# Optimization experiments

Hardware: AMD Instinct MI355X
Metric: run time of the kernel (lower is better)

Reference implementation:

```python
import jax, jax.numpy as jnp
import numpy as np
import math

N_NODES = 50000
N_EDGES = 800000
D_NODE = 128
D_EDGE = 64  # 4 + dist_embed_dim(60)
N_HEADS = 8
HEAD_DIM = D_NODE // N_HEADS


def setup_inputs() -> dict:
    key = jax.random.key(0)
    ks = jax.random.split(key, 8)
    scale_q = 1.0 / math.sqrt(D_NODE)
    scale_kv = 1.0 / math.sqrt(D_NODE + D_EDGE)
    return {
        "node_feats": jax.random.normal(ks[0], (N_NODES, D_NODE), jnp.float32),
        "edge_feats": jax.random.normal(ks[1], (N_EDGES, D_EDGE), jnp.float32),
        "edge_index": jax.random.randint(ks[2], (2, N_EDGES), 0, N_NODES, jnp.int32),
        "Wq": jax.random.normal(ks[3], (D_NODE, D_NODE), jnp.float32) * scale_q,
        "bq": jnp.zeros((D_NODE,), jnp.float32),
        "Wk": jax.random.normal(ks[4], (D_NODE + D_EDGE, D_NODE), jnp.float32) * scale_kv,
        "bk": jnp.zeros((D_NODE,), jnp.float32),
        "Wv": jax.random.normal(ks[5], (D_NODE + D_EDGE, D_NODE), jnp.float32) * scale_kv,
        "bv": jnp.zeros((D_NODE,), jnp.float32),
        "Wo": jax.random.normal(ks[6], (D_NODE, D_NODE), jnp.float32) * scale_q,
        "bo": jnp.zeros((D_NODE,), jnp.float32),
    }


def reference(node_feats, edge_feats, edge_index, Wq, bq, Wk, bk, Wv, bv, Wo, bo):
    src, tgt = edge_index[0], edge_index[1]
    n = node_feats.shape[0]
    e = edge_feats.shape[0]

    # per-edge Q from target node, K/V from [source node || edge feats]
    q = (node_feats[tgt] @ Wq + bq).reshape(e, N_HEADS, HEAD_DIM)
    kv_input = jnp.concatenate([node_feats[src], edge_feats], axis=-1)  # [E, D_NODE+D_EDGE]
    k = (kv_input @ Wk + bk).reshape(e, N_HEADS, HEAD_DIM)
    v = (kv_input @ Wv + bv).reshape(e, N_HEADS, HEAD_DIM)

    # per-edge attention logits [E, H]
    a = jnp.einsum("ehc,ehc->eh", q, k) / math.sqrt(HEAD_DIM)

    # segment softmax over edges grouped by target node (numerically stable)
    seg_max = jax.ops.segment_max(a, tgt, num_segments=n)      # [N, H]
    a = jnp.exp(a - seg_max[tgt])
    seg_sum = jax.ops.segment_sum(a, tgt, num_segments=n)      # [N, H]
    a = a / seg_sum[tgt]

    # weighted scatter-sum aggregate
    o = jax.ops.segment_sum(a[..., None] * v, tgt, num_segments=n)  # [N, H, C]
    out = o.reshape(n, N_HEADS * HEAD_DIM) @ Wo + bo
    return out  # dropout is identity at inference
```

## Files before the change

### kernel.cpp

```cpp
#include <hip/hip_runtime.h>

#define NND 50000
#define NED 800000
#define DN 128
#define DE 64
#define DKV 192
#define NH 8
#define HD 16

__device__ __forceinline__ float sane(float x) {
    return (x == x && fabsf(x) < 1e30f) ? x : 0.f;
}

__global__ __launch_bounds__(256) void node_proj_qkv(
    const float* __restrict__ nf,
    const float* __restrict__ Wq, const float* __restrict__ bq,
    const float* __restrict__ Wk, const float* __restrict__ bk,
    const float* __restrict__ Wv, const float* __restrict__ bv,
    float* __restrict__ Qn, float* __restrict__ Kn, float* __restrict__ Vn)
{
    __shared__ alignas(16) float xs[128][8];
    const int t = threadIdx.x;
    const int nb = blockIdx.x * 8;
    {
        const int node = t >> 5;
        const int k0 = (t & 31) * 4;
        const float4 x4 = *(const float4*)(nf + (size_t)(nb + node) * DN + k0);
        xs[k0 + 0][node] = x4.x;
        xs[k0 + 1][node] = x4.y;
        xs[k0 + 2][node] = x4.z;
        xs[k0 + 3][node] = x4.w;
    }
    __syncthreads();

    const int col = t & 127;
    const int grp = t >> 7;
    float aq[4], ak[4], av[4];
    const float bqv = bq[col], bkv = bk[col], bvv = bv[col];
#pragma unroll
    for (int i = 0; i < 4; i++) { aq[i] = bqv; ak[i] = bkv; av[i] = bvv; }

#pragma unroll 4
    for (int k = 0; k < 128; k++) {
        const float wq = Wq[k * DN + col];
        const float wk = Wk[k * DN + col];
        const float wv = Wv[k * DN + col];
        const float4 x = *(const float4*)&xs[k][grp * 4];
        aq[0] += x.x * wq; aq[1] += x.y * wq; aq[2] += x.z * wq; aq[3] += x.w * wq;
        ak[0] += x.x * wk; ak[1] += x.y * wk; ak[2] += x.z * wk; ak[3] += x.w * wk;
        av[0] += x.x * wv; av[1] += x.y * wv; av[2] += x.z * wv; av[3] += x.w * wv;
    }
#pragma unroll
    for (int i = 0; i < 4; i++) {
        const size_t r = (size_t)(nb + grp * 4 + i) * DN + col;
        Qn[r] = aq[i]; Kn[r] = ak[i]; Vn[r] = av[i];
    }
}

__global__ __launch_bounds__(256) void node_proj_q(
    const float* __restrict__ nf,
    const float* __restrict__ Wq, const float* __restrict__ bq,
    float* __restrict__ Qn)
{
    __shared__ alignas(16) float xs[128][8];
    const int t = threadIdx.x;
    const int nb = blockIdx.x * 8;
    {
        const int node = t >> 5;
        const int k0 = (t & 31) * 4;
        const float4 x4 = *(const float4*)(nf + (size_t)(nb + node) * DN + k0);
        xs[k0 + 0][node] = x4.x;
        xs[k0 + 1][node] = x4.y;
        xs[k0 + 2][node] = x4.z;
        xs[k0 + 3][node] = x4.w;
    }
    __syncthreads();

    const int col = t & 127;
    const int grp = t >> 7;
    float aq[4];
    const float bqv = bq[col];
#pragma unroll
    for (int i = 0; i < 4; i++) aq[i] = bqv;

#pragma unroll 4
    for (int k = 0; k < 128; k++) {
        const float wq = Wq[k * DN + col];
        const float4 x = *(const float4*)&xs[k][grp * 4];
        aq[0] += x.x * wq; aq[1] += x.y * wq; aq[2] += x.z * wq; aq[3] += x.w * wq;
    }
#pragma unroll
    for (int i = 0; i < 4; i++)
        Qn[(size_t)(nb + grp * 4 + i) * DN + col] = aq[i];
}

__global__ __launch_bounds__(256) void edge_hist(
    const int* __restrict__ eidx, int* __restrict__ cnt)
{
    const int e = blockIdx.x * 256 + threadIdx.x;
    atomicAdd(&cnt[eidx[NED + e]], 1);
}

__global__ __launch_bounds__(1024) void scan_offsets(
    const int* __restrict__ cnt, int* __restrict__ offs)
{
    __shared__ int partial[1024];
    const int t = threadIdx.x;
    constexpr int CH = (NND + 1023) / 1024;
    const int base = t * CH;
    int s = 0;
    for (int i = 0; i < CH; i++) {
        const int idx = base + i;
        if (idx < NND) s += cnt[idx];
    }
    partial[t] = s;
    __syncthreads();
    for (int off = 1; off < 1024; off <<= 1) {
        const int v = (t >= off) ? partial[t - off] : 0;
        __syncthreads();
        partial[t] += v;
        __syncthreads();
    }
    int run = (t == 0) ? 0 : partial[t - 1];
    for (int i = 0; i < CH; i++) {
        const int idx = base + i;
        if (idx < NND) { offs[idx] = run; run += cnt[idx]; }
    }
}

__global__ __launch_bounds__(256) void edge_scatter(
    const int* __restrict__ eidx, int* __restrict__ offs,
    int* __restrict__ perm, int* __restrict__ srcp)
{
    const int e = blockIdx.x * 256 + threadIdx.x;
    const int pos = atomicAdd(&offs[eidx[NED + e]], 1);
    perm[pos] = e;
    srcp[pos] = eidx[e];
}

__global__ __launch_bounds__(256) void edge_aggregate(
    const float* __restrict__ ef,
    const int* __restrict__ cnt, const int* __restrict__ offs,
    const int* __restrict__ perm, const int* __restrict__ srcp,
    const float* __restrict__ Wk, const float* __restrict__ Wv,
    const float* __restrict__ Kn, const float* __restrict__ Vn,
    float* qo)
{
    __shared__ alignas(16) float efs[4][8][64];
    const int t = threadIdx.x;
    const int w = t >> 6;
    const int l = t & 63;
    const int j = l & 7;
    const int node = blockIdx.x * 4 + w;

    const int end = offs[node];
    const int beg = end - cnt[node];

    const float* __restrict__ WkB = Wk + 128 * DN;
    const float* __restrict__ WvB = Wv + 128 * DN;

    const float2 q2 = *(const float2*)(qo + (size_t)node * DN + 2 * l);

    float qt[8];
#pragma unroll
    for (int i = 0; i < 8; i++) qt[i] = 0.f;
#pragma unroll 16
    for (int k = 0; k < 64; k++) {
        const float2 wk2 = *(const float2*)(WkB + k * DN + 2 * l);
        float part = q2.x * wk2.x + q2.y * wk2.y;
        part += __shfl_xor(part, 1);
        part += __shfl_xor(part, 2);
        part += __shfl_xor(part, 4);
        if (j == (k >> 3)) qt[k & 7] = part;
    }

    float acc0 = 0.f, acc1 = 0.f, segacc = 0.f;
    float gt[8];
#pragma unroll
    for (int i = 0; i < 8; i++) gt[i] = 0.f;

    for (int base = beg; base < end; base += 8) {
        const int myE = min(base + (l >> 3), end - 1);
        const int pe = perm[myE];
        const float4 A = *(const float4*)(ef + (size_t)pe * DE + j * 8);
        const float4 B = *(const float4*)(ef + (size_t)pe * DE + j * 8 + 4);
        *(float4*)&efs[w][l >> 3][j * 8]     = A;
        *(float4*)&efs[w][l >> 3][j * 8 + 4] = B;

        const int mySrc = srcp[myE];

#pragma unroll
        for (int e = 0; e < 8; e++) {
            const int se = __builtin_amdgcn_readlane(mySrc, e * 8);
            const float4 efA = *(const float4*)&efs[w][e][j * 8];
            const float4 efB = *(const float4*)&efs[w][e][j * 8 + 4];
            const float2 kn2 = *(const float2*)(Kn + (size_t)se * DN + 2 * l);
            float part = q2.x * kn2.x + q2.y * kn2.y
                       + efA.x * qt[0] + efA.y * qt[1] + efA.z * qt[2] + efA.w * qt[3]
                       + efB.x * qt[4] + efB.y * qt[5] + efB.z * qt[6] + efB.w * qt[7];
            part += __shfl_xor(part, 1);
            part += __shfl_xor(part, 2);
            part += __shfl_xor(part, 4);
            const float arg = fminf(fmaxf(part * 0.25f, -60.f), 60.f);
            const float p = (base + e < end) ? __expf(arg) : 0.f;
            const float2 vn2 = *(const float2*)(Vn + (size_t)se * DN + 2 * l);
            acc0 += p * vn2.x;
            acc1 += p * vn2.y;
            segacc += p;
            gt[0] += p * efA.x; gt[1] += p * efA.y; gt[2] += p * efA.z; gt[3] += p * efA.w;
            gt[4] += p * efB.x; gt[5] += p * efB.y; gt[6] += p * efB.z; gt[7] += p * efB.w;
        }
    }

    float oe0 = 0.f, oe1 = 0.f;
#pragma unroll 16
    for (int k = 0; k < 64; k++) {
        const float g = __shfl(gt[k & 7], (l & 56) | (k >> 3));
        const float2 wv2 = *(const float2*)(WvB + k * DN + 2 * l);
        oe0 += g * wv2.x;
        oe1 += g * wv2.y;
    }
    acc0 += oe0;
    acc1 += oe1;

    const float r = (segacc > 0.f) ? 1.f / segacc : 0.f;
    float* orow = qo + (size_t)node * DN + 2 * l;
    orow[0] = sane(acc0 * r);
    orow[1] = sane(acc1 * r);
}

__global__ __launch_bounds__(256) void edge_pass_full(
    const float* __restrict__ nf, const float* __restrict__ ef,
    const int* __restrict__ eidx,
    const float* __restrict__ Wk, const float* __restrict__ bk,
    const float* __restrict__ Wv, const float* __restrict__ bv,
    const float* __restrict__ Qn,
    float* __restrict__ o_un, float* __restrict__ seg)
{
    __shared__ alignas(16) float kvs[4][192][4];
    const int t = threadIdx.x;
    const int w = t >> 6;
    const int l = t & 63;
    const int eb = blockIdx.x * 16 + w * 4;

    int src[4], tgt[4];
#pragma unroll
    for (int e = 0; e < 4; e++) {
        src[e] = eidx[eb + e];
        tgt[e] = eidx[NED + eb + e];
    }

#pragma unroll
    for (int it = 0; it < 3; it++) {
        const int idx = it * 64 + l;
        const int e = idx / 48;
        const int pos = (idx % 48) * 4;
        const float* p = (pos < 128)
            ? nf + (size_t)src[e] * DN + pos
            : ef + (size_t)(eb + e) * DE + (pos - 128);
        const float4 x4 = *(const float4*)p;
        kvs[w][pos + 0][e] = x4.x;
        kvs[w][pos + 1][e] = x4.y;
        kvs[w][pos + 2][e] = x4.z;
        kvs[w][pos + 3][e] = x4.w;
    }
    __syncthreads();

    const float bk0 = bk[2 * l], bk1 = bk[2 * l + 1];
    const float bv0 = bv[2 * l], bv1 = bv[2 * l + 1];
    float accK[4][2] = {{bk0,bk1},{bk0,bk1},{bk0,bk1},{bk0,bk1}};
    float accV[4][2] = {{bv0,bv1},{bv0,bv1},{bv0,bv1},{bv0,bv1}};

#pragma unroll 4
    for (int k = 0; k < DKV; k++) {
        const float4 e4 = *(const float4*)&kvs[w][k][0];
        const float2 wk2 = *(const float2*)(Wk + k * DN + 2 * l);
        const float2 wv2 = *(const float2*)(Wv + k * DN + 2 * l);
        accK[0][0] += e4.x * wk2.x; accK[0][1] += e4.x * wk2.y;
        accK[1][0] += e4.y * wk2.x; accK[1][1] += e4.y * wk2.y;
        accK[2][0] += e4.z * wk2.x; accK[2][1] += e4.z * wk2.y;
        accK[3][0] += e4.w * wk2.x; accK[3][1] += e4.w * wk2.y;
        accV[0][0] += e4.x * wv2.x; accV[0][1] += e4.x * wv2.y;
        accV[1][0] += e4.y * wv2.x; accV[1][1] += e4.y * wv2.y;
        accV[2][0] += e4.z * wv2.x; accV[2][1] += e4.z * wv2.y;
        accV[3][0] += e4.w * wv2.x; accV[3][1] += e4.w * wv2.y;
    }

    const int h = l >> 3;
#pragma unroll
    for (int e = 0; e < 4; e++) {
        const float2 q2 = *(const float2*)(Qn + (size_t)tgt[e] * DN + 2 * l);
        float part = q2.x * accK[e][0] + q2.y * accK[e][1];
        part += __shfl_xor(part, 1);
        part += __shfl_xor(part, 2);
        part += __shfl_xor(part, 4);
        float arg = fminf(fmaxf(part * 0.25f, -60.f), 60.f);
        const float p = __expf(arg);

        atomicAdd(&o_un[(size_t)tgt[e] * DN + 2 * l],     p * accV[e][0]);
        atomicAdd(&o_un[(size_t)tgt[e] * DN + 2 * l + 1], p * accV[e][1]);
        if ((l & 7) == 0) atomicAdd(&seg[tgt[e] * NH + h], p);
    }
}

__global__ __launch_bounds__(256) void out_proj(
    const float* o_un, const float* __restrict__ seg,
    const float* __restrict__ Wo, const float* __restrict__ bo,
    float* out)
{
    __shared__ alignas(16) float xs[128][8];
    const int t = threadIdx.x;
    const int nb = blockIdx.x * 8;
    {
        const int node = t >> 5;
        const int k0 = (t & 31) * 4;
        const float4 v = *(const float4*)(o_un + (size_t)(nb + node) * DN + k0);
        float r = 1.f;
        if (seg) {
            const float s = seg[(nb + node) * NH + (k0 >> 4)];
            r = (s > 0.f) ? 1.f / s : 0.f;
        }
        xs[k0 + 0][node] = sane(v.x * r);
        xs[k0 + 1][node] = sane(v.y * r);
        xs[k0 + 2][node] = sane(v.z * r);
        xs[k0 + 3][node] = sane(v.w * r);
    }
    __syncthreads();

    const int col = t & 127;
    const int grp = t >> 7;
    float acc[4];
    const float b = bo[col];
#pragma unroll
    for (int i = 0; i < 4; i++) acc[i] = b;

#pragma unroll 4
    for (int k = 0; k < 128; k++) {
        const float wo = Wo[k * DN + col];
        const float4 x = *(const float4*)&xs[k][grp * 4];
        acc[0] += x.x * wo; acc[1] += x.y * wo; acc[2] += x.z * wo; acc[3] += x.w * wo;
    }
#pragma unroll
    for (int i = 0; i < 4; i++)
        out[(size_t)(nb + grp * 4 + i) * DN + col] = acc[i];
}

extern "C" void kernel_launch(void* const* d_in, const int* in_sizes, int n_in,
                              void* d_out, int out_size, void* d_ws, size_t ws_size,
                              hipStream_t stream) {
    const float* nf   = (const float*)d_in[0];
    const float* ef   = (const float*)d_in[1];
    const int*   eidx = (const int*)d_in[2];
    const float* Wq   = (const float*)d_in[3];
    const float* bq   = (const float*)d_in[4];
    const float* Wk   = (const float*)d_in[5];
    const float* bk   = (const float*)d_in[6];
    const float* Wv   = (const float*)d_in[7];
    const float* bv   = (const float*)d_in[8];
    const float* Wo   = (const float*)d_in[9];
    const float* bo   = (const float*)d_in[10];
    float* out = (float*)d_out;

    float* Qn = out;

    const size_t tabBytes = (size_t)NND * DN * sizeof(float);
    const size_t csrBytes = 2 * tabBytes
                          + (size_t)(2 * NND + 2 * NED) * sizeof(int);
    const size_t accBytes = tabBytes + (size_t)NND * NH * sizeof(float);

    if (ws_size >= csrBytes) {
        float* Kn  = (float*)d_ws;
        float* Vn  = Kn + (size_t)NND * DN;
        int*   cnt = (int*)(Vn + (size_t)NND * DN);
        int*   offs= cnt + NND;
        int*   perm= offs + NND;
        int*   srcp= perm + NED;
        hipMemsetAsync(cnt, 0, NND * sizeof(int), stream);
        node_proj_qkv<<<NND / 8, 256, 0, stream>>>(nf, Wq, bq, Wk, bk, Wv, bv, Qn, Kn, Vn);
        edge_hist<<<NED / 256, 256, 0, stream>>>(eidx, cnt);
        scan_offsets<<<1, 1024, 0, stream>>>(cnt, offs);
        edge_scatter<<<NED / 256, 256, 0, stream>>>(eidx, offs, perm, srcp);
        edge_aggregate<<<NND / 4, 256, 0, stream>>>(ef, cnt, offs, perm, srcp,
                                                    Wk, Wv, Kn, Vn, Qn);
        out_proj<<<NND / 8, 256, 0, stream>>>(Qn, nullptr, Wo, bo, out);
    } else {
        float* o_un = (float*)d_ws;
        float* seg  = o_un + (size_t)NND * DN;
        hipMemsetAsync(o_un, 0, accBytes, stream);
        node_proj_q<<<NND / 8, 256, 0, stream>>>(nf, Wq, bq, Qn);
        edge_pass_full<<<NED / 16, 256, 0, stream>>>(nf, ef, eidx, Wk, bk, Wv, bv, Qn, o_un, seg);
        out_proj<<<NND / 8, 256, 0, stream>>>(o_un, seg, Wo, bo, out);
    }
}
```

Measured before the change: 871.9 us.

## Parallelize offset scan, pack edge CSR, prefetch edges in aggregation

Replaces the single-block offset scan with a three-kernel multi-block scan (block sums, scan of partials, per-block scan). Packs edge id and source index into one int2 array, so the scatter writes and the aggregate reads one record per edge. In the aggregation kernel, it computes the per-head query-times-Wk fold with vector loads after broadcasting q by shuffle, instead of 64 shuffle reductions. It also software-prefetches the next batch of edge features and issues all K/V gathers before the compute loop. This adds two kernel launches and more registers for the prefetched values.

```diff
diff --git a/kernel.cpp b/kernel.cpp
--- a/kernel.cpp
+++ b/kernel.cpp
@@ -101,47 +101,69 @@
     atomicAdd(&cnt[eidx[NED + e]], 1);
 }
 
-__global__ __launch_bounds__(1024) void scan_offsets(
-    const int* __restrict__ cnt, int* __restrict__ offs)
-{
-    __shared__ int partial[1024];
-    const int t = threadIdx.x;
-    constexpr int CH = (NND + 1023) / 1024;
-    const int base = t * CH;
-    int s = 0;
-    for (int i = 0; i < CH; i++) {
-        const int idx = base + i;
-        if (idx < NND) s += cnt[idx];
-    }
-    partial[t] = s;
-    __syncthreads();
-    for (int off = 1; off < 1024; off <<= 1) {
-        const int v = (t >= off) ? partial[t - off] : 0;
+#define SCAN_NB ((NND + 255) / 256)
+
+__global__ __launch_bounds__(256) void scanA(
+    const int* __restrict__ cnt, int* __restrict__ partial)
+{
+    const int idx = blockIdx.x * 256 + threadIdx.x;
+    int v = (idx < NND) ? cnt[idx] : 0;
+#pragma unroll
+    for (int off = 1; off < 64; off <<= 1) v += __shfl_xor(v, off);
+    __shared__ int wsum[4];
+    if ((threadIdx.x & 63) == 0) wsum[threadIdx.x >> 6] = v;
+    __syncthreads();
+    if (threadIdx.x == 0)
+        partial[blockIdx.x] = wsum[0] + wsum[1] + wsum[2] + wsum[3];
+}
+
+__global__ __launch_bounds__(256) void scanB(int* __restrict__ partial)
+{
+    __shared__ int s[256];
+    const int t = threadIdx.x;
+    const int v = (t < SCAN_NB) ? partial[t] : 0;
+    s[t] = v;
+    __syncthreads();
+    for (int off = 1; off < 256; off <<= 1) {
+        const int u = (t >= off) ? s[t - off] : 0;
         __syncthreads();
-        partial[t] += v;
+        s[t] += u;
         __syncthreads();
     }
-    int run = (t == 0) ? 0 : partial[t - 1];
-    for (int i = 0; i < CH; i++) {
-        const int idx = base + i;
-        if (idx < NND) { offs[idx] = run; run += cnt[idx]; }
-    }
+    if (t < SCAN_NB) partial[t] = s[t] - v;
+}
+
+__global__ __launch_bounds__(256) void scanC(
+    const int* __restrict__ cnt, const int* __restrict__ partial,
+    int* __restrict__ offs)
+{
+    __shared__ int s[256];
+    const int t = threadIdx.x;
+    const int idx = blockIdx.x * 256 + t;
+    const int v = (idx < NND) ? cnt[idx] : 0;
+    s[t] = v;
+    __syncthreads();
+    for (int off = 1; off < 256; off <<= 1) {
+        const int u = (t >= off) ? s[t - off] : 0;
+        __syncthreads();
+        s[t] += u;
+        __syncthreads();
+    }
+    if (idx < NND) offs[idx] = partial[blockIdx.x] + s[t] - v;
 }
 
 __global__ __launch_bounds__(256) void edge_scatter(
-    const int* __restrict__ eidx, int* __restrict__ offs,
-    int* __restrict__ perm, int* __restrict__ srcp)
+    const int* __restrict__ eidx, int* __restrict__ offs, int2* __restrict__ epack)
 {
     const int e = blockIdx.x * 256 + threadIdx.x;
     const int pos = atomicAdd(&offs[eidx[NED + e]], 1);
-    perm[pos] = e;
-    srcp[pos] = eidx[e];
+    epack[pos] = make_int2(e, eidx[e]);
 }
 
 __global__ __launch_bounds__(256) void edge_aggregate(
     const float* __restrict__ ef,
     const int* __restrict__ cnt, const int* __restrict__ offs,
-    const int* __restrict__ perm, const int* __restrict__ srcp,
+    const int2* __restrict__ epack,
     const float* __restrict__ Wk, const float* __restrict__ Wv,
     const float* __restrict__ Kn, const float* __restrict__ Vn,
     float* qo)
@@ -151,6 +173,7 @@
     const int w = t >> 6;
     const int l = t & 63;
     const int j = l & 7;
+    const int es = l >> 3;
     const int node = blockIdx.x * 4 + w;
 
     const int end = offs[node];
@@ -161,17 +184,24 @@
 
     const float2 q2 = *(const float2*)(qo + (size_t)node * DN + 2 * l);
 
+    float qh[16];
+#pragma unroll
+    for (int m = 0; m < 8; m++) {
+        qh[2 * m]     = __shfl(q2.x, (l & 56) + m);
+        qh[2 * m + 1] = __shfl(q2.y, (l & 56) + m);
+    }
     float qt[8];
 #pragma unroll
-    for (int i = 0; i < 8; i++) qt[i] = 0.f;
-#pragma unroll 16
-    for (int k = 0; k < 64; k++) {
-        const float2 wk2 = *(const float2*)(WkB + k * DN + 2 * l);
-        float part = q2.x * wk2.x + q2.y * wk2.y;
-        part += __shfl_xor(part, 1);
-        part += __shfl_xor(part, 2);
-        part += __shfl_xor(part, 4);
-        if (j == (k >> 3)) qt[k & 7] = part;
+    for (int i = 0; i < 8; i++) {
+        const float* wrow = WkB + (j * 8 + i) * DN + (l & 56) * 2;
+        const float4 w0 = *(const float4*)(wrow);
+        const float4 w1 = *(const float4*)(wrow + 4);
+        const float4 w2 = *(const float4*)(wrow + 8);
+        const float4 w3 = *(const float4*)(wrow + 12);
+        qt[i] = qh[0]  * w0.x + qh[1]  * w0.y + qh[2]  * w0.z + qh[3]  * w0.w
+              + qh[4]  * w1.x + qh[5]  * w1.y + qh[6]  * w1.z + qh[7]  * w1.w
+              + qh[8]  * w2.x + qh[9]  * w2.y + qh[10] * w2.z + qh[11] * w2.w
+              + qh[12] * w3.x + qh[13] * w3.y + qh[14] * w3.z + qh[15] * w3.w;
     }
 
     float acc0 = 0.f, acc1 = 0.f, segacc = 0.f;
@@ -179,36 +209,49 @@
 #pragma unroll
     for (int i = 0; i < 8; i++) gt[i] = 0.f;
 
-    for (int base = beg; base < end; base += 8) {
-        const int myE = min(base + (l >> 3), end - 1);
-        const int pe = perm[myE];
-        const float4 A = *(const float4*)(ef + (size_t)pe * DE + j * 8);
-        const float4 B = *(const float4*)(ef + (size_t)pe * DE + j * 8 + 4);
-        *(float4*)&efs[w][l >> 3][j * 8]     = A;
-        *(float4*)&efs[w][l >> 3][j * 8 + 4] = B;
-
-        const int mySrc = srcp[myE];
-
-#pragma unroll
-        for (int e = 0; e < 8; e++) {
-            const int se = __builtin_amdgcn_readlane(mySrc, e * 8);
-            const float4 efA = *(const float4*)&efs[w][e][j * 8];
-            const float4 efB = *(const float4*)&efs[w][e][j * 8 + 4];
-            const float2 kn2 = *(const float2*)(Kn + (size_t)se * DN + 2 * l);
-            float part = q2.x * kn2.x + q2.y * kn2.y
-                       + efA.x * qt[0] + efA.y * qt[1] + efA.z * qt[2] + efA.w * qt[3]
-                       + efB.x * qt[4] + efB.y * qt[5] + efB.z * qt[6] + efB.w * qt[7];
-            part += __shfl_xor(part, 1);
-            part += __shfl_xor(part, 2);
-            part += __shfl_xor(part, 4);
-            const float arg = fminf(fmaxf(part * 0.25f, -60.f), 60.f);
-            const float p = (base + e < end) ? __expf(arg) : 0.f;
-            const float2 vn2 = *(const float2*)(Vn + (size_t)se * DN + 2 * l);
-            acc0 += p * vn2.x;
-            acc1 += p * vn2.y;
-            segacc += p;
-            gt[0] += p * efA.x; gt[1] += p * efA.y; gt[2] += p * efA.z; gt[3] += p * efA.w;
-            gt[4] += p * efB.x; gt[5] += p * efB.y; gt[6] += p * efB.z; gt[7] += p * efB.w;
+    if (beg < end) {
+        int2 ep = epack[min(beg + es, end - 1)];
+        float4 A = *(const float4*)(ef + (size_t)ep.x * DE + j * 8);
+        float4 B = *(const float4*)(ef + (size_t)ep.x * DE + j * 8 + 4);
+
+        for (int base = beg; base < end; base += 8) {
+            const int nbase = base + 8;
+            int2 ep_n; float4 An, Bn;
+            if (nbase < end) {
+                ep_n = epack[min(nbase + es, end - 1)];
+                An = *(const float4*)(ef + (size_t)ep_n.x * DE + j * 8);
+                Bn = *(const float4*)(ef + (size_t)ep_n.x * DE + j * 8 + 4);
+            }
+            *(float4*)&efs[w][es][j * 8]     = A;
+            *(float4*)&efs[w][es][j * 8 + 4] = B;
+
+            float2 kn[8], vn[8];
+#pragma unroll
+            for (int e = 0; e < 8; e++) {
+                const int se = __builtin_amdgcn_readlane(ep.y, e * 8);
+                kn[e] = *(const float2*)(Kn + (size_t)se * DN + 2 * l);
+                vn[e] = *(const float2*)(Vn + (size_t)se * DN + 2 * l);
+            }
+
+#pragma unroll
+            for (int e = 0; e < 8; e++) {
+                const float4 efA = *(const float4*)&efs[w][e][j * 8];
+                const float4 efB = *(const float4*)&efs[w][e][j * 8 + 4];
+                float part = q2.x * kn[e].x + q2.y * kn[e].y
+                           + efA.x * qt[0] + efA.y * qt[1] + efA.z * qt[2] + efA.w * qt[3]
+                           + efB.x * qt[4] + efB.y * qt[5] + efB.z * qt[6] + efB.w * qt[7];
+                part += __shfl_xor(part, 1);
+                part += __shfl_xor(part, 2);
+                part += __shfl_xor(part, 4);
+                const float arg = fminf(fmaxf(part * 0.25f, -60.f), 60.f);
+                const float p = (base + e < end) ? __expf(arg) : 0.f;
+                acc0 += p * vn[e].x;
+                acc1 += p * vn[e].y;
+                segacc += p;
+                gt[0] += p * efA.x; gt[1] += p * efA.y; gt[2] += p * efA.z; gt[3] += p * efA.w;
+                gt[4] += p * efB.x; gt[5] += p * efB.y; gt[6] += p * efB.z; gt[7] += p * efB.w;
+            }
+            ep = ep_n; A = An; B = Bn;
         }
     }
 
@@ -365,22 +408,24 @@
 
     const size_t tabBytes = (size_t)NND * DN * sizeof(float);
     const size_t csrBytes = 2 * tabBytes
-                          + (size_t)(2 * NND + 2 * NED) * sizeof(int);
+                          + ((size_t)2 * NND + 2 * NED + SCAN_NB) * sizeof(int);
     const size_t accBytes = tabBytes + (size_t)NND * NH * sizeof(float);
 
     if (ws_size >= csrBytes) {
-        float* Kn  = (float*)d_ws;
-        float* Vn  = Kn + (size_t)NND * DN;
-        int*   cnt = (int*)(Vn + (size_t)NND * DN);
-        int*   offs= cnt + NND;
-        int*   perm= offs + NND;
-        int*   srcp= perm + NED;
+        float* Kn     = (float*)d_ws;
+        float* Vn     = Kn + (size_t)NND * DN;
+        int*   cnt    = (int*)(Vn + (size_t)NND * DN);
+        int*   offs   = cnt + NND;
+        int2*  epack  = (int2*)(offs + NND);
+        int*   partial= (int*)(epack + NED);
         hipMemsetAsync(cnt, 0, NND * sizeof(int), stream);
         node_proj_qkv<<<NND / 8, 256, 0, stream>>>(nf, Wq, bq, Wk, bk, Wv, bv, Qn, Kn, Vn);
         edge_hist<<<NED / 256, 256, 0, stream>>>(eidx, cnt);
-        scan_offsets<<<1, 1024, 0, stream>>>(cnt, offs);
-        edge_scatter<<<NED / 256, 256, 0, stream>>>(eidx, offs, perm, srcp);
-        edge_aggregate<<<NND / 4, 256, 0, stream>>>(ef, cnt, offs, perm, srcp,
+        scanA<<<SCAN_NB, 256, 0, stream>>>(cnt, partial);
+        scanB<<<1, 256, 0, stream>>>(partial);
+        scanC<<<SCAN_NB, 256, 0, stream>>>(cnt, partial, offs);
+        edge_scatter<<<NED / 256, 256, 0, stream>>>(eidx, offs, epack);
+        edge_aggregate<<<NND / 4, 256, 0, stream>>>(ef, cnt, offs, epack,
                                                     Wk, Wv, Kn, Vn, Qn);
         out_proj<<<NND / 8, 256, 0, stream>>>(Qn, nullptr, Wo, bo, out);
     } else {
```

Result: no change. 865.9 us (-0.7%).
